# Kernel optimization log

Measured on AMD Instinct MI355X. Metric: run time of the kernel, lower is better.

## Reference

```python
import jax, jax.numpy as jnp
import numpy as np

B = 8192
N_IN = 1024
N_OUT = 1024
IN_OUT = N_IN + N_OUT


def setup_inputs() -> dict:
    key = jax.random.key(0)
    ks = jax.random.split(key, 11)
    s = 1.0 / np.sqrt(IN_OUT)  # nn.Linear default init scale
    inp = {
        "x": jax.random.normal(ks[0], (B, N_IN), dtype=jnp.float32),
        "out_tm1": jax.random.normal(ks[1], (B, N_OUT), dtype=jnp.float32),
        "state_tm1": jax.random.normal(ks[2], (B, N_OUT), dtype=jnp.float32),
        "Wf": jax.random.uniform(ks[3], (IN_OUT, N_OUT), jnp.float32, -s, s),
        "bf": jax.random.uniform(ks[4], (N_OUT,), jnp.float32, -s, s),
        "Wi": jax.random.uniform(ks[5], (IN_OUT, N_OUT), jnp.float32, -s, s),
        "bi": jax.random.uniform(ks[6], (N_OUT,), jnp.float32, -s, s),
        "Wc": jax.random.uniform(ks[7], (IN_OUT, N_OUT), jnp.float32, -s, s),
        "bc": jax.random.uniform(ks[8], (N_OUT,), jnp.float32, -s, s),
        "Wo": jax.random.uniform(ks[9], (IN_OUT, N_OUT), jnp.float32, -s, s),
        "bo": jax.random.uniform(ks[10], (N_OUT,), jnp.float32, -s, s),
    }
    return inp


def reference(x, out_tm1, state_tm1, Wf, bf, Wi, bi, Wc, bc, Wo, bo):
    xh = jnp.concatenate((x, out_tm1), axis=-1)  # [B, n_in+n_out]
    f = jax.nn.sigmoid(xh @ Wf + bf)             # forget gate
    i = jax.nn.sigmoid(xh @ Wi + bi)             # input gate
    c = jnp.tanh(xh @ Wc + bc)                   # candidates
    o = jax.nn.sigmoid(xh @ Wo + bo)             # output gate
    new_state = state_tm1 * f + i * c
    output_t = o * jnp.tanh(new_state)
    return (output_t, new_state)
```

## Files before the change

kernel.cpp:

```cpp
#include <hip/hip_runtime.h>

#define B_DIM 8192
#define NOUT  1024
#define KDIM  2048

typedef __bf16 bf16x8 __attribute__((ext_vector_type(8)));
typedef float  f32x4  __attribute__((ext_vector_type(4)));

__device__ __forceinline__ unsigned short f2bf(float f) {
  unsigned int u = __float_as_uint(f);
  u += 0x7fff + ((u >> 16) & 1);
  return (unsigned short)(u >> 16);
}
__device__ __forceinline__ float sigmoid_f(float x) {
  return 1.0f / (1.0f + __expf(-x));
}
__device__ __forceinline__ float tanh_f(float x) {
  return 1.0f - 2.0f / (__expf(2.0f * x) + 1.0f);
}
__device__ __forceinline__ void gload_lds16(const void* g, void* l) {
  __builtin_amdgcn_global_load_lds(
      (const __attribute__((address_space(1))) void*)g,
      (__attribute__((address_space(3))) void*)l, 16, 0, 0);
}

__device__ __forceinline__ int cimap(int g, int n) {
  return ((n >> 6) << 8) | ((g >> 1) << 7) | (((n >> 4) & 3) << 5) |
         ((g & 1) << 4) | (n & 15);
}

__global__ void pack_xh_kernel(const float* __restrict__ x,
                               const float* __restrict__ h,
                               unsigned short* __restrict__ xh) {
  const long total = (long)B_DIM * KDIM / 4;
  for (long i = (long)blockIdx.x * blockDim.x + threadIdx.x; i < total;
       i += (long)gridDim.x * blockDim.x) {
    long e = i * 4;
    int b = (int)(e >> 11);
    int c = (int)(e & 2047);
    float4 v = (c < 1024)
        ? *reinterpret_cast<const float4*>(x + (long)b * 1024 + c)
        : *reinterpret_cast<const float4*>(h + (long)b * 1024 + (c - 1024));
    ushort4 o;
    o.x = f2bf(v.x); o.y = f2bf(v.y); o.z = f2bf(v.z); o.w = f2bf(v.w);
    *reinterpret_cast<ushort4*>(xh + e) = o;
  }
}

__global__ void transpose_w_kernel(const float* __restrict__ Wf,
                                   const float* __restrict__ Wi,
                                   const float* __restrict__ Wc,
                                   const float* __restrict__ Wo,
                                   unsigned short* __restrict__ wt) {
  __shared__ float tile[32][33];
  const int g = blockIdx.z;
  const float* W = (g == 0) ? Wf : (g == 1) ? Wi : (g == 2) ? Wc : Wo;
  const int n0 = blockIdx.x * 32;
  const int k0 = blockIdx.y * 32;
  const int tx = threadIdx.x, ty = threadIdx.y;
#pragma unroll
  for (int r = ty; r < 32; r += 8)
    tile[r][tx] = W[(long)(k0 + r) * NOUT + n0 + tx];
  __syncthreads();
#pragma unroll
  for (int r = ty; r < 32; r += 8) {
    int ci = cimap(g, n0 + r);
    wt[(long)ci * KDIM + k0 + tx] = f2bf(tile[tx][r]);
  }
}

#define BAR()   { __builtin_amdgcn_s_barrier(); __builtin_amdgcn_sched_barrier(0); }
#define VM6()   { asm volatile("s_waitcnt vmcnt(6)" ::: "memory"); }
#define VM4()   { asm volatile("s_waitcnt vmcnt(4)" ::: "memory"); }
#define VM0()   { asm volatile("s_waitcnt vmcnt(0)" ::: "memory"); }

__device__ __forceinline__ void stage_half(const char* g, long grow0, int kt,
                                           char* ldsm, int base,
                                           int wave, int lane) {
  const int rsub = lane >> 3;
  const int scol = (((lane & 7) ^ rsub) << 4);
  const long rowb = (grow0 + wave * 8 + rsub) * 4096 + (long)kt * 128 + scol;
  gload_lds16(g + rowb,               ldsm + base + wave * 1024);
  gload_lds16(g + rowb + 64L * 4096,  ldsm + base + 8192 + wave * 1024);
}

#define LOAD_AF(BUF, MQ)                                                    \
  _Pragma("unroll") for (int mi = 0; mi < 4; ++mi) {                        \
    af[mi][0] = *reinterpret_cast<const bf16x8*>(                           \
        baseA0 + (BUF)*32768 + (MQ)*16384 + mi*2048);                       \
    af[mi][1] = *reinterpret_cast<const bf16x8*>(                           \
        baseA1 + (BUF)*32768 + (MQ)*16384 + mi*2048);                       \
  }

#define LOAD_BQ(BUF, NQ, DST)                                               \
  _Pragma("unroll") for (int ni = 0; ni < 2; ++ni) {                        \
    DST[ni][0] = *reinterpret_cast<const bf16x8*>(                          \
        baseB0 + (BUF)*32768 + (NQ)*16384 + ni*2048);                       \
    DST[ni][1] = *reinterpret_cast<const bf16x8*>(                          \
        baseB1 + (BUF)*32768 + (NQ)*16384 + ni*2048);                       \
  }

#define MFMA16(MQ, NQ, BQ)                                                  \
  __builtin_amdgcn_s_setprio(1);                                            \
  _Pragma("unroll") for (int mi = 0; mi < 4; ++mi)                          \
  _Pragma("unroll") for (int ni = 0; ni < 2; ++ni)                          \
  _Pragma("unroll") for (int s = 0; s < 2; ++s)                             \
    acc[MQ][NQ][mi][ni] = __builtin_amdgcn_mfma_f32_16x16x32_bf16(          \
        af[mi][s], BQ[ni][s], acc[MQ][NQ][mi][ni], 0, 0, 0);                \
  __builtin_amdgcn_s_setprio(0);

__global__ __launch_bounds__(512, 2)
void lstm_gemm_kernel(const unsigned short* __restrict__ xh,
                      const unsigned short* __restrict__ wt,
                      const float* __restrict__ state,
                      const float* __restrict__ bfp,
                      const float* __restrict__ bip,
                      const float* __restrict__ bcp,
                      const float* __restrict__ bop,
                      float* __restrict__ out) {
  __shared__ __attribute__((aligned(128))) char lds[131072];

  const int tid  = threadIdx.x;
  const int wave = tid >> 6;
  const int lane = tid & 63;
  const int wm = wave >> 2;
  const int wn = wave & 3;

  int wg = blockIdx.y * 16 + blockIdx.x;
  wg = (wg & 7) * 64 + (wg >> 3);
  const int  bm = wg >> 4;
  const int  bn = wg & 15;
  const long m0 = (long)bm * 256;
  const long n0 = (long)bn * 256;

  const int lrow  = lane & 15;
  const int csw   = (lane & 7) << 4;
  const int ck    = (lane >> 4) << 4;
  const int colA0 = ck ^ csw;
  const int colA1 = (64 | ck) ^ csw;

  const char* baseA0 = lds + (wm * 64 + lrow) * 128 + colA0;
  const char* baseA1 = lds + (wm * 64 + lrow) * 128 + colA1;
  const char* baseB0 = lds + 65536 + (wn * 32 + lrow) * 128 + colA0;
  const char* baseB1 = lds + 65536 + (wn * 32 + lrow) * 128 + colA1;

  const char* xh_b = (const char*)xh;
  const char* wt_b = (const char*)wt;

  stage_half(xh_b, m0,        0, lds, 0,                     wave, lane);
  stage_half(wt_b, n0,        0, lds, 65536,                 wave, lane);
  stage_half(wt_b, n0 + 128,  0, lds, 65536 + 16384,         wave, lane);
  stage_half(xh_b, m0 + 128,  0, lds, 16384,                 wave, lane);
  stage_half(xh_b, m0,        1, lds, 32768,                 wave, lane);
  stage_half(wt_b, n0,        1, lds, 65536 + 32768,         wave, lane);

  f32x4 acc[2][2][4][2] = {};
  bf16x8 af[4][2];
  bf16x8 bq0[2][2];
  bf16x8 bq1[2][2];

  VM4();
  BAR();

  for (int t = 0; t < 32; t += 2) {
    const int k2c = (t + 2 > 31) ? 31 : t + 2;
    const int k3c = (t + 3 > 31) ? 31 : t + 3;

    LOAD_AF(0, 0) LOAD_BQ(0, 0, bq0)
    stage_half(wt_b, n0 + 128, t + 1, lds, 65536 + 32768 + 16384, wave, lane);
    VM6(); BAR();
    MFMA16(0, 0, bq0)
    LOAD_BQ(0, 1, bq1)
    stage_half(xh_b, m0 + 128, t + 1, lds, 32768 + 16384, wave, lane);
    VM6(); BAR();
    MFMA16(0, 1, bq1)
    LOAD_AF(0, 1)
    stage_half(xh_b, m0, k2c, lds, 0, wave, lane);
    VM6(); BAR();
    MFMA16(1, 1, bq1)
    stage_half(wt_b, n0, k2c, lds, 65536, wave, lane);
    VM6(); BAR();
    MFMA16(1, 0, bq0)

    LOAD_AF(1, 0) LOAD_BQ(1, 0, bq0)
    stage_half(wt_b, n0 + 128, k2c, lds, 65536 + 16384, wave, lane);
    VM6(); BAR();
    MFMA16(0, 0, bq0)
    LOAD_BQ(1, 1, bq1)
    stage_half(xh_b, m0 + 128, k2c, lds, 16384, wave, lane);
    VM6(); BAR();
    MFMA16(0, 1, bq1)
    LOAD_AF(1, 1)
    stage_half(xh_b, m0, k3c, lds, 32768, wave, lane);
    VM6(); BAR();
    MFMA16(1, 1, bq1)
    stage_half(wt_b, n0, k3c, lds, 65536 + 32768, wave, lane);
    VM6(); BAR();
    MFMA16(1, 0, bq0)
  }
  VM0();

  const int   nout = bn * 64 + wn * 16 + lrow;
  const int   rsub4 = (lane >> 4) << 2;
  const float bfv = bfp[nout], biv = bip[nout];
  const float bcv = bcp[nout], bov = bop[nout];
  float* out2 = out + (long)B_DIM * NOUT;
#pragma unroll
  for (int mq = 0; mq < 2; ++mq)
#pragma unroll
    for (int mi = 0; mi < 4; ++mi)
#pragma unroll
      for (int v = 0; v < 4; ++v) {
        const long row = m0 + mq * 128 + wm * 64 + mi * 16 + rsub4 + v;
        float fg = sigmoid_f(acc[mq][0][mi][0][v] + bfv);
        float ig = sigmoid_f(acc[mq][0][mi][1][v] + biv);
        float cg = tanh_f   (acc[mq][1][mi][0][v] + bcv);
        float og = sigmoid_f(acc[mq][1][mi][1][v] + bov);
        float st = state[row * NOUT + nout];
        float ns = st * fg + ig * cg;
        out [row * NOUT + nout] = og * tanh_f(ns);
        out2[row * NOUT + nout] = ns;
      }
}

extern "C" void kernel_launch(void* const* d_in, const int* in_sizes, int n_in,
                              void* d_out, int out_size, void* d_ws, size_t ws_size,
                              hipStream_t stream) {
  const float* x     = (const float*)d_in[0];
  const float* h     = (const float*)d_in[1];
  const float* state = (const float*)d_in[2];
  const float* Wf    = (const float*)d_in[3];
  const float* bfp   = (const float*)d_in[4];
  const float* Wi    = (const float*)d_in[5];
  const float* bip   = (const float*)d_in[6];
  const float* Wc    = (const float*)d_in[7];
  const float* bcp   = (const float*)d_in[8];
  const float* Wo    = (const float*)d_in[9];
  const float* bop   = (const float*)d_in[10];
  float* out = (float*)d_out;

  unsigned short* xh = (unsigned short*)d_ws;
  unsigned short* wt = (unsigned short*)((char*)d_ws + (size_t)B_DIM * KDIM * 2);

  hipLaunchKernelGGL(pack_xh_kernel, dim3(2048), dim3(256), 0, stream, x, h, xh);
  hipLaunchKernelGGL(transpose_w_kernel, dim3(NOUT / 32, KDIM / 32, 4),
                     dim3(32, 8), 0, stream, Wf, Wi, Wc, Wo, wt);
  hipLaunchKernelGGL(lstm_gemm_kernel, dim3(16, 32), dim3(512), 0, stream,
                     xh, wt, state, bfp, bip, bcp, bop, out);
}
```

Baseline: 153.3 us.

## Restructure GEMM main loop into two barriers per k-tile with bulk staging

Reworks the software pipeline in the LSTM GEMM main loop. Each k-tile now uses two barrier phases instead of four, with three stage_half loads issued up front, the fourth issued after the first MFMA half, and wait thresholds of vmcnt(6)/vmcnt(2). The prologue prefetch depth drops from six half-tiles to four, and setprio now wraps pairs of MFMA groups. The aim is to cut barrier count and sync overhead. In exchange, less global-load latency is hidden because the prefetch runs only one tile ahead instead of roughly two.

After: 153.1 us. Within noise of the previous version (-0.1%).

```diff
diff --git a/kernel.cpp b/kernel.cpp
--- a/kernel.cpp
+++ b/kernel.cpp
@@ -71,7 +71,7 @@
 
 #define BAR()   { __builtin_amdgcn_s_barrier(); __builtin_amdgcn_sched_barrier(0); }
 #define VM6()   { asm volatile("s_waitcnt vmcnt(6)" ::: "memory"); }
-#define VM4()   { asm volatile("s_waitcnt vmcnt(4)" ::: "memory"); }
+#define VM2()   { asm volatile("s_waitcnt vmcnt(2)" ::: "memory"); }
 #define VM0()   { asm volatile("s_waitcnt vmcnt(0)" ::: "memory"); }
 
 __device__ __forceinline__ void stage_half(const char* g, long grow0, int kt,
@@ -101,13 +101,11 @@
   }
 
 #define MFMA16(MQ, NQ, BQ)                                                  \
-  __builtin_amdgcn_s_setprio(1);                                            \
   _Pragma("unroll") for (int mi = 0; mi < 4; ++mi)                          \
   _Pragma("unroll") for (int ni = 0; ni < 2; ++ni)                          \
   _Pragma("unroll") for (int s = 0; s < 2; ++s)                             \
     acc[MQ][NQ][mi][ni] = __builtin_amdgcn_mfma_f32_16x16x32_bf16(          \
-        af[mi][s], BQ[ni][s], acc[MQ][NQ][mi][ni], 0, 0, 0);                \
-  __builtin_amdgcn_s_setprio(0);
+        af[mi][s], BQ[ni][s], acc[MQ][NQ][mi][ni], 0, 0, 0);
 
 __global__ __launch_bounds__(512, 2)
 void lstm_gemm_kernel(const unsigned short* __restrict__ xh,
@@ -147,56 +145,52 @@
   const char* xh_b = (const char*)xh;
   const char* wt_b = (const char*)wt;
 
-  stage_half(xh_b, m0,        0, lds, 0,                     wave, lane);
-  stage_half(wt_b, n0,        0, lds, 65536,                 wave, lane);
-  stage_half(wt_b, n0 + 128,  0, lds, 65536 + 16384,         wave, lane);
-  stage_half(xh_b, m0 + 128,  0, lds, 16384,                 wave, lane);
-  stage_half(xh_b, m0,        1, lds, 32768,                 wave, lane);
-  stage_half(wt_b, n0,        1, lds, 65536 + 32768,         wave, lane);
+  stage_half(xh_b, m0,        0, lds, 0,             wave, lane);
+  stage_half(wt_b, n0,        0, lds, 65536,         wave, lane);
+  stage_half(wt_b, n0 + 128,  0, lds, 65536 + 16384, wave, lane);
+  stage_half(xh_b, m0 + 128,  0, lds, 16384,         wave, lane);
 
   f32x4 acc[2][2][4][2] = {};
   bf16x8 af[4][2];
   bf16x8 bq0[2][2];
   bf16x8 bq1[2][2];
 
-  VM4();
+  VM0();
   BAR();
 
   for (int t = 0; t < 32; t += 2) {
+    const int k1  = t + 1;
     const int k2c = (t + 2 > 31) ? 31 : t + 2;
-    const int k3c = (t + 3 > 31) ? 31 : t + 3;
-
-    LOAD_AF(0, 0) LOAD_BQ(0, 0, bq0)
-    stage_half(wt_b, n0 + 128, t + 1, lds, 65536 + 32768 + 16384, wave, lane);
+
+    stage_half(xh_b, m0,       k1, lds, 32768,         wave, lane);
+    stage_half(wt_b, n0,       k1, lds, 65536 + 32768, wave, lane);
+    stage_half(wt_b, n0 + 128, k1, lds, 65536 + 32768 + 16384, wave, lane);
+    LOAD_AF(0, 0) LOAD_BQ(0, 0, bq0) LOAD_BQ(0, 1, bq1)
     VM6(); BAR();
-    MFMA16(0, 0, bq0)
-    LOAD_BQ(0, 1, bq1)
-    stage_half(xh_b, m0 + 128, t + 1, lds, 32768 + 16384, wave, lane);
+    __builtin_amdgcn_s_setprio(1);
+    MFMA16(0, 0, bq0) MFMA16(0, 1, bq1)
+    __builtin_amdgcn_s_setprio(0);
+    stage_half(xh_b, m0 + 128, k1, lds, 32768 + 16384, wave, lane);
+    LOAD_AF(0, 1)
+    VM2(); BAR();
+    __builtin_amdgcn_s_setprio(1);
+    MFMA16(1, 1, bq1) MFMA16(1, 0, bq0)
+    __builtin_amdgcn_s_setprio(0);
+
+    stage_half(xh_b, m0,       k2c, lds, 0,             wave, lane);
+    stage_half(wt_b, n0,       k2c, lds, 65536,         wave, lane);
+    stage_half(wt_b, n0 + 128, k2c, lds, 65536 + 16384, wave, lane);
+    LOAD_AF(1, 0) LOAD_BQ(1, 0, bq0) LOAD_BQ(1, 1, bq1)
     VM6(); BAR();
-    MFMA16(0, 1, bq1)
-    LOAD_AF(0, 1)
-    stage_half(xh_b, m0, k2c, lds, 0, wave, lane);
-    VM6(); BAR();
-    MFMA16(1, 1, bq1)
-    stage_half(wt_b, n0, k2c, lds, 65536, wave, lane);
-    VM6(); BAR();
-    MFMA16(1, 0, bq0)
-
-    LOAD_AF(1, 0) LOAD_BQ(1, 0, bq0)
-    stage_half(wt_b, n0 + 128, k2c, lds, 65536 + 16384, wave, lane);
-    VM6(); BAR();
-    MFMA16(0, 0, bq0)
-    LOAD_BQ(1, 1, bq1)
+    __builtin_amdgcn_s_setprio(1);
+    MFMA16(0, 0, bq0) MFMA16(0, 1, bq1)
+    __builtin_amdgcn_s_setprio(0);
     stage_half(xh_b, m0 + 128, k2c, lds, 16384, wave, lane);
-    VM6(); BAR();
-    MFMA16(0, 1, bq1)
     LOAD_AF(1, 1)
-    stage_half(xh_b, m0, k3c, lds, 32768, wave, lane);
-    VM6(); BAR();
-    MFMA16(1, 1, bq1)
-    stage_half(wt_b, n0, k3c, lds, 65536 + 32768, wave, lane);
-    VM6(); BAR();
-    MFMA16(1, 0, bq0)
+    VM2(); BAR();
+    __builtin_amdgcn_s_setprio(1);
+    MFMA16(1, 1, bq1) MFMA16(1, 0, bq0)
+    __builtin_amdgcn_s_setprio(0);
   }
   VM0();
 
```
